# Optimization experiments

Hardware: AMD Instinct MI355X
Metric: run time of the kernel (lower is better)

Reference implementation:

```python
import jax, jax.numpy as jnp
import numpy as np

PI = 3.141592653589793


def conv2d(x, w, b=None, padding=0, groups=1):
    out = jax.lax.conv_general_dilated(
        x, w, window_strides=(1, 1), padding=((padding, padding), (padding, padding)),
        dimension_numbers=('NCHW', 'OIHW', 'NCHW'), feature_group_count=groups)
    if b is not None:
        out = out + b.reshape(1, -1, 1, 1)
    return out


def group_norm(x, weight, bias, num_groups, eps=1e-5):
    B, C, H, W = x.shape
    xg = x.reshape(B, num_groups, C // num_groups, H, W)
    mean = xg.mean(axis=(2, 3, 4), keepdims=True)
    var = xg.var(axis=(2, 3, 4), keepdims=True)
    xg = (xg - mean) / jnp.sqrt(var + eps)
    return xg.reshape(B, C, H, W) * weight.reshape(1, -1, 1, 1) + bias.reshape(1, -1, 1, 1)


def l2norm(x, eps=1e-12):
    n = jnp.sqrt(jnp.sum(x * x, axis=1, keepdims=True))
    return x / jnp.maximum(n, eps)


def dense_sift(x):
    # kornia DenseSIFTDescriptor defaults: 8 angle bins, 4x4 spatial bins, bin size 4,
    # stride 1, padding 1, rootsift=True, clipval=0.2. Input (B,1,H,W) -> (B,128,H,W).
    eps = 1e-10
    B, C, H, W = x.shape
    # spatial_gradient(x, 'diff'), normalized: central differences / 2, replicate pad
    p = jnp.pad(x, ((0, 0), (0, 0), (1, 1), (1, 1)), mode='edge')
    gx = (p[:, :, 1:-1, 2:] - p[:, :, 1:-1, :-2]) * 0.5
    gy = (p[:, :, 2:, 1:-1] - p[:, :, :-2, 1:-1]) * 0.5
    mag = jnp.sqrt(gx * gx + gy * gy + eps)
    ori = jnp.arctan2(gy, gx + eps) + 2.0 * PI
    o_big = 8.0 * ori / (2.0 * PI)
    bo0f = jnp.floor(o_big)
    wo1 = o_big - bo0f
    bo0 = bo0f % 8
    bo1 = (bo0 + 1) % 8
    wo0m = (1.0 - wo1) * mag
    wo1m = wo1 * mag
    bins = jnp.arange(8, dtype=x.dtype).reshape(1, 8, 1, 1)
    # soft orientation-histogram binning -> (B,8,H,W)
    ang = jnp.where(bo0 == bins, wo0m, 0.0) + jnp.where(bo1 == bins, wo1m, 0.0)
    # triangular bin pooling kernel (ksize=4), depthwise conv, pad 2 -> (B,8,H+1,W+1)
    ks2 = 2.0
    xc2 = ks2 - jnp.abs(jnp.arange(4, dtype=x.dtype) + 0.5 - ks2)
    pk = jnp.outer(xc2, xc2) / (ks2 ** 2)
    pk = jnp.tile(pk.reshape(1, 1, 4, 4), (8, 1, 1, 1))
    pooled = jax.lax.conv_general_dilated(
        ang, pk, (1, 1), ((2, 2), (2, 2)),
        dimension_numbers=('NCHW', 'OIHW', 'NCHW'), feature_group_count=8)
    # PoolingConv with identity reshape kernel (k=4, pad=1) == 4x4 patch extraction
    pp = jnp.pad(pooled, ((0, 0), (0, 0), (1, 1), (1, 1)))
    patches = jnp.stack([pp[:, :, y:y + H, xx:xx + W]
                         for y in range(4) for xx in range(4)], axis=2)  # (B,8,16,H,W)
    out = patches.reshape(B, 128, H, W)
    out = jnp.clip(l2norm(out), 0.0, 0.2)
    out = l2norm(out)
    # rootsift: sqrt(L1-normalized + eps)
    l1 = jnp.sum(jnp.abs(out), axis=1, keepdims=True)
    out = jnp.sqrt(out / jnp.maximum(l1, 1e-12) + eps)
    return out


def gauss1d(ks, sigma):
    t = jnp.arange(ks, dtype=jnp.float32) - (ks - 1) / 2.0
    g = jnp.exp(-(t * t) / (2.0 * sigma * sigma))
    return g / g.sum()


def joint_bilateral_blur(inp, guidance, ks=5, sigma_color=0.1, sigma_space=(1.5, 1.5)):
    # kornia joint_bilateral_blur: border_type='reflect', color_distance_type='l1'
    B, C, H, W = inp.shape
    pad = ks // 2
    pi_ = jnp.pad(inp, ((0, 0), (0, 0), (pad, pad), (pad, pad)), mode='reflect')
    pg = jnp.pad(guidance, ((0, 0), (0, 0), (pad, pad), (pad, pad)), mode='reflect')

    def unfold(p):  # (B,C,H,W,ks*ks), flatten order (dy, dx)
        return jnp.stack([p[:, :, y:y + H, x:x + W]
                          for y in range(ks) for x in range(ks)], axis=-1)

    ui = unfold(pi_)
    ug = unfold(pg)
    diff = ug - guidance[..., None]
    cdist_sq = jnp.square(jnp.sum(jnp.abs(diff), axis=1, keepdims=True))  # L1 over channels, squared
    color_k = jnp.exp(-0.5 / (sigma_color ** 2) * cdist_sq)               # (B,1,H,W,K2)
    space_k = jnp.outer(gauss1d(ks, sigma_space[0]), gauss1d(ks, sigma_space[1])).reshape(1, 1, 1, 1, -1)
    kernel = space_k * color_k
    return (ui * kernel).sum(-1) / kernel.sum(-1)


def setup_inputs() -> dict:
    key = jax.random.key(0)
    ks = jax.random.split(key, 8)
    B, H, W = 4, 270, 512

    def wgt(k, shape, scale=0.05):
        return jax.random.normal(k, shape, dtype=jnp.float32) * scale

    z = lambda n: jnp.zeros((n,), dtype=jnp.float32)
    o = lambda n: jnp.ones((n,), dtype=jnp.float32)
    return {
        'x': jax.random.normal(ks[0], (B, 1, H, W), dtype=jnp.float32),
        'w1': wgt(ks[1], (64, 128, 5, 5)), 'b1': z(64), 'g1w': o(64), 'g1b': z(64),
        'w2': wgt(ks[2], (32, 64, 3, 3)), 'b2': z(32), 'g2w': o(32), 'g2b': z(32),
        'w3': wgt(ks[3], (16, 32, 3, 3)), 'b3': z(16), 'g3w': o(16), 'g3b': z(16),
        'w4': wgt(ks[4], (8, 16, 3, 3)), 'b4': z(8), 'g4w': o(8), 'g4b': z(8),
        'w5': wgt(ks[5], (2, 8, 3, 3)), 'b5': z(2),
        'sw1': wgt(ks[6], (32, 128, 1, 1)), 'sb1': z(32),
        'sw2': wgt(ks[7], (8, 32, 1, 1)), 'sb2': z(8),
    }


def reference(x, w1, b1, g1w, g1b, w2, b2, g2w, g2b, w3, b3, g3w, g3b,
              w4, b4, g4w, g4b, w5, b5, sw1, sb1, sw2, sb2):
    orig = x
    s = dense_sift(x)                                     # (B,128,H,W)
    h = jax.nn.relu(group_norm(conv2d(s, w1, b1, 2), g1w, g1b, 8))
    h = jax.nn.relu(group_norm(conv2d(h, w2, b2, 1), g2w, g2b, 8))
    h = h + conv2d(s, sw1, sb1, 0)                        # skip 1
    blk = h
    h = jax.nn.relu(group_norm(conv2d(h, w3, b3, 1), g3w, g3b, 4))
    h = jax.nn.relu(group_norm(conv2d(h, w4, b4, 1), g4w, g4b, 4))
    h = h + conv2d(blk, sw2, sb2, 0)                      # skip 2
    h = conv2d(h, w5, b5, 1)                              # (B,2,H,W)
    guide = jnp.tile(orig, (1, 2, 1, 1))
    h = joint_bilateral_blur(h, guide, ks=5, sigma_color=0.1, sigma_space=(1.5, 1.5))
    h = jnp.tanh(h)
    scale = jnp.array([0.436, 0.615], dtype=h.dtype).reshape(1, 2, 1, 1)
    return h * scale
```

## Files before the change

### kernel.cpp

```cpp
#include <hip/hip_runtime.h>

#define DEV __device__ __forceinline__

typedef __bf16 bf16x8 __attribute__((ext_vector_type(8)));
typedef float f32x4 __attribute__((ext_vector_type(4)));

union U8 { uint4 q; unsigned short u[8]; };

constexpr int BN = 4, H = 270, W = 512, HW = H * W;
constexpr int IH5 = 274, P5 = 516;
constexpr int IH3 = 272, P3 = 514;

DEV unsigned short f2bf(float f) {
  unsigned int u = __builtin_bit_cast(unsigned int, f);
  u = (u + 0x7FFFu + ((u >> 16) & 1u)) >> 16;
  return (unsigned short)u;
}
DEV float bf2f(unsigned short h) {
  return __builtin_bit_cast(float, (unsigned int)h << 16);
}

#define GLL16(g, l)                                                                        \
  __builtin_amdgcn_global_load_lds((const __attribute__((address_space(1))) void*)(g),     \
                                   (__attribute__((address_space(3))) void*)(l), 16, 0, 0)

DEV int swz(int row) { return ((row >> 1) & 3) << 4; }

__global__ void k_fill(float* __restrict__ out, int n, float v) {
  int i = blockIdx.x * 256 + threadIdx.x;
  if (i < n) out[i] = v;
}

template <int C, int PD>
__global__ void k_halo(unsigned short* __restrict__ buf, int IHt, int pitch, int nb_) {
  int vPerRow = pitch * C / 8;
  int topBot = 2 * PD * vPerRow;
  int sideV = PD * C / 8;
  int midRows = IHt - 2 * PD;
  int perS = topBot + midRows * 2 * sideV;
  int v = blockIdx.x * 256 + threadIdx.x;
  if (v >= nb_ * perS) return;
  int s = v / perS, r = v % perS;
  size_t base = (size_t)s * IHt * pitch * C;
  size_t off;
  if (r < topBot) {
    int half = r / (PD * vPerRow);
    int rr = r % (PD * vPerRow);
    off = ((size_t)(half ? (IHt - PD) : 0) * pitch * C) + (size_t)rr * 8;
  } else {
    int r2 = r - topBot;
    int row = r2 / (2 * sideV), c2 = r2 % (2 * sideV);
    int side = c2 / sideV, cc = c2 % sideV;
    off = ((size_t)(PD + row) * pitch + (side ? (pitch - PD) : 0)) * C + (size_t)cc * 8;
  }
  *(uint4*)(buf + base + off) = uint4{0, 0, 0, 0};
}

__global__ void k_sift_ang(const float* __restrict__ x, float* __restrict__ ang, int nTot) {
  int p = blockIdx.x * 256 + threadIdx.x;
  if (p >= nTot) return;
  int b = p / HW, r = p % HW, y = r / W, xx = r % W;
  const float* xb = x + (size_t)b * HW;
  float xm = xb[y * W + (xx > 0 ? xx - 1 : 0)];
  float xp = xb[y * W + (xx < W - 1 ? xx + 1 : W - 1)];
  float ym = xb[(y > 0 ? y - 1 : 0) * W + xx];
  float yp = xb[(y < H - 1 ? y + 1 : H - 1) * W + xx];
  float gx = (xp - xm) * 0.5f, gy = (yp - ym) * 0.5f;
  float mag = sqrtf(gx * gx + gy * gy + 1e-10f);
  float ori = atan2f(gy, gx + 1e-10f) + 6.2831855f;
  float o = (8.0f * ori) / 6.2831855f;
  float bo0f = floorf(o);
  float wo1 = o - bo0f;
  int b0 = ((int)bo0f) & 7;
  int b1 = (b0 + 1) & 7;
  float w0m = (1.0f - wo1) * mag, w1m = wo1 * mag;
  float v[8];
#pragma unroll
  for (int k = 0; k < 8; ++k)
    v[k] = (k == b0 ? w0m : 0.0f) + (k == b1 ? w1m : 0.0f);
  float4* o4 = (float4*)(ang + (size_t)p * 8);
  o4[0] = make_float4(v[0], v[1], v[2], v[3]);
  o4[1] = make_float4(v[4], v[5], v[6], v[7]);
}

__global__ void k_sift_pool(const float* __restrict__ ang, float* __restrict__ pooled, int nTot) {
  constexpr int PH = H + 1, PW = W + 1;
  int p = blockIdx.x * 256 + threadIdx.x;
  if (p >= nTot) return;
  int b = p / (PH * PW), r = p % (PH * PW), y = r / PW, xx = r % PW;
  float4 a0 = {0, 0, 0, 0}, a1 = {0, 0, 0, 0};
  const float xc2[4] = {0.5f, 1.5f, 1.5f, 0.5f};
#pragma unroll
  for (int ky = 0; ky < 4; ++ky) {
    int yy = y - 2 + ky;
    if (yy < 0 || yy >= H) continue;
#pragma unroll
    for (int kx = 0; kx < 4; ++kx) {
      int xs = xx - 2 + kx;
      if (xs < 0 || xs >= W) continue;
      float w = xc2[ky] * xc2[kx] * 0.25f;
      const float4* s4 = (const float4*)(ang + ((size_t)(b * H + yy) * W + xs) * 8);
      float4 v0 = s4[0], v1 = s4[1];
      a0.x += w * v0.x; a0.y += w * v0.y; a0.z += w * v0.z; a0.w += w * v0.w;
      a1.x += w * v1.x; a1.y += w * v1.y; a1.z += w * v1.z; a1.w += w * v1.w;
    }
  }
  float4* o4 = (float4*)(pooled + (size_t)p * 8);
  o4[0] = a0; o4[1] = a1;
}

__global__ void k_sift_desc(const float* __restrict__ pooled, unsigned short* __restrict__ spad) {
  constexpr int PH = H + 1, PW = W + 1;
  int tid = threadIdx.x;
  int wv = tid >> 6, lane = tid & 63;
  int p = blockIdx.x * 4 + wv;
  int b = p / HW, r = p % HW, yy = r / W, xx = r % W;
  int a = lane >> 3, jj = lane & 7;
  int j0 = jj * 2;
  int dy = j0 >> 2, dx = j0 & 3;
  int rr = yy + dy - 1;
  int c0 = xx + dx - 1, c1 = c0 + 1;
  bool rv = (rr >= 0 && rr <= H);
  int rc = min(max(rr, 0), H);
  const float* pb = pooled + ((size_t)(b * PH + rc) * PW) * 8 + a;
  float v0 = 0.0f, v1 = 0.0f;
  if (rv && c0 >= 0 && c0 <= W) v0 = pb[(size_t)c0 * 8];
  if (rv && c1 >= 0 && c1 <= W) v1 = pb[(size_t)c1 * 8];

  float n2 = v0 * v0 + v1 * v1;
#pragma unroll
  for (int m = 1; m < 64; m <<= 1) n2 += __shfl_xor(n2, m);
  float inv = 1.0f / fmaxf(sqrtf(n2), 1e-12f);
  v0 = fminf(v0 * inv, 0.2f);
  v1 = fminf(v1 * inv, 0.2f);
  float S = v0 + v1;
#pragma unroll
  for (int m = 1; m < 64; m <<= 1) S += __shfl_xor(S, m);
  float iS = 1.0f / fmaxf(S, 1e-12f);
  v0 = sqrtf(v0 * iS + 1e-10f);
  v1 = sqrtf(v1 * iS + 1e-10f);
  unsigned int pk = (unsigned int)f2bf(v0) | ((unsigned int)f2bf(v1) << 16);
  *(unsigned int*)(spad + ((size_t)(b * IH5 + yy + 2) * P5 + xx + 2) * 128 + lane * 2) = pk;
}

template <int CIN, int COUT, int KS>
__global__ void k_prep(const float* __restrict__ w, unsigned short* __restrict__ wbuf) {
  int i = blockIdx.x * 256 + threadIdx.x;
  if (i >= KS * KS * COUT * CIN) return;
  int t = i / (COUT * CIN), r2 = i % (COUT * CIN), co = r2 / CIN, e = r2 % CIN;
  wbuf[i] = f2bf(w[(co * CIN + e) * (KS * KS) + t]);
}

DEV int xcd_remap(int bid, int nbid) {
  int q8 = nbid >> 3, r8 = nbid & 7;
  int xcd = bid & 7;
  return (xcd < r8 ? xcd * (q8 + 1) : r8 * (q8 + 1) + (xcd - r8) * q8) + (bid >> 3);
}

template <int CIN, int COUT, int KS, int NG, int MINW, bool FSKIP, int BMPX>
__launch_bounds__(BMPX, MINW)
__global__ void k_convr(const unsigned short* __restrict__ in, int IHt, int ipitch,
                        const unsigned short* __restrict__ wtap,
                        const float* __restrict__ bias,
                        const unsigned short* __restrict__ wsk,
                        const float* __restrict__ skb,
                        unsigned short* __restrict__ outraw,
                        unsigned short* __restrict__ skraw,
                        float* __restrict__ part, int nbid) {
  constexpr int NWV = BMPX / 64;
  constexpr int NXB = 512 / BMPX;
  constexpr int SLABPX = BMPX + KS - 1;
  constexpr int KQ = CIN / 32;
  constexpr int NF = COUT / 16;
  constexpr int SLAB = SLABPX * 64;
  constexpr int SWQ = COUT * 64;
  constexpr int SWROW = KS * SWQ;
  constexpr int SSK = FSKIP ? 32 * 64 : 16;
  constexpr int STRIDE = BMPX * 16;
  __shared__ __align__(16) unsigned char slabB[2][SLAB];
  __shared__ __align__(16) unsigned char wrowB[2][SWROW];
  __shared__ __align__(16) unsigned char wskB[2][SSK];
  __shared__ float red[NWV][16];

  int tid = threadIdx.x;
  int lane = tid & 63, wid = tid >> 6;
  int l15 = lane & 15, hi = lane >> 4;

  int byl = xcd_remap(blockIdx.x, nbid);
  int half = byl % NXB, rowid = byl / NXB;
  int y = rowid % H, b = rowid / H;
  int x0 = half * BMPX;

  f32x4 acc[4][NF] = {};
  f32x4 ask[4][2] = {};

  auto stage = [&](int it, int pbuf) {
    int q = it / KS, ky = it % KS;
    const char* src = (const char*)(in + ((size_t)(b * IHt + y + ky) * ipitch + x0) * CIN + q * 32);
    for (int d = tid * 16; d < SLAB; d += STRIDE) {
      int px = d >> 6, qb = d & 63;
      GLL16(src + px * (CIN * 2) + (qb ^ swz(px)), slabB[pbuf] + d);
    }
    const char* wsrc = (const char*)wtap + (size_t)(ky * KS) * (COUT * CIN * 2) + q * 64;
    for (int d = tid * 16; d < SWROW; d += STRIDE) {
      int kx = d / SWQ, rem = d % SWQ;
      int co = rem >> 6, qb = rem & 63;
      GLL16(wsrc + (size_t)kx * (COUT * CIN * 2) + co * (CIN * 2) + (qb ^ swz(co)), wrowB[pbuf] + d);
    }
  };
  auto stage_wsk = [&](int q, int pbuf) {
    const char* src = (const char*)wsk + q * 64;
    for (int d = tid * 16; d < 32 * 64; d += STRIDE) {
      int co = d >> 6, qb = d & 63;
      GLL16(src + co * (CIN * 2) + (qb ^ swz(co)), wskB[pbuf] + d);
    }
  };

  stage(0, 0);
  if constexpr (FSKIP) stage_wsk(0, 0);
  __syncthreads();

#pragma unroll 1
  for (int it = 0; it < KQ * KS; ++it) {
    int cur = it & 1;
    int q = it / KS, ky = it % KS;
    if (it + 1 < KQ * KS) {
      stage(it + 1, cur ^ 1);
      if (FSKIP && (it + 1) % KS == 0) stage_wsk((it + 1) / KS, ((it + 1) / KS) & 1);
    }
    const unsigned char* sl = slabB[cur];
    const unsigned char* wr = wrowB[cur];
    int koff = hi * 16;
#pragma unroll
    for (int kx = 0; kx < KS; ++kx) {
      bf16x8 af[4];
#pragma unroll
      for (int mi = 0; mi < 4; ++mi) {
        int px = wid * 64 + mi * 16 + l15 + kx;
        af[mi] = *(const bf16x8*)(sl + px * 64 + (koff ^ swz(px)));
      }
#pragma unroll
      for (int ni = 0; ni < NF; ++ni) {
        int co = ni * 16 + l15;
        bf16x8 bq = *(const bf16x8*)(wr + kx * SWQ + co * 64 + (koff ^ swz(co)));
#pragma unroll
        for (int mi = 0; mi < 4; ++mi)
          acc[mi][ni] = __builtin_amdgcn_mfma_f32_16x16x32_bf16(af[mi], bq, acc[mi][ni], 0, 0, 0);
      }
      if constexpr (FSKIP) {
        if (ky == KS / 2 && kx == KS / 2) {
#pragma unroll
          for (int ni = 0; ni < 2; ++ni) {
            int co = ni * 16 + l15;
            bf16x8 bq = *(const bf16x8*)(wskB[q & 1] + co * 64 + (koff ^ swz(co)));
#pragma unroll
            for (int mi = 0; mi < 4; ++mi)
              ask[mi][ni] = __builtin_amdgcn_mfma_f32_16x16x32_bf16(af[mi], bq, ask[mi][ni], 0, 0, 0);
          }
        }
      }
    }
    __syncthreads();
  }

#pragma unroll
  for (int ni = 0; ni < NF; ++ni) {
    float bv = bias[ni * 16 + l15];
#pragma unroll
    for (int mi = 0; mi < 4; ++mi)
#pragma unroll
      for (int rr = 0; rr < 4; ++rr)
        acc[mi][ni][rr] += bv;
  }
  unsigned short* op = outraw + ((size_t)(b * H + y) * W + x0) * COUT;
#pragma unroll
  for (int mi = 0; mi < 4; ++mi)
#pragma unroll
    for (int rr = 0; rr < 4; ++rr) {
      int px = wid * 64 + mi * 16 + hi * 4 + rr;
#pragma unroll
      for (int ni = 0; ni < NF; ++ni)
        op[(size_t)px * COUT + ni * 16 + l15] = f2bf(acc[mi][ni][rr]);
    }
  if constexpr (FSKIP) {
    unsigned short* ops = skraw + ((size_t)(b * H + y) * W + x0) * 32;
#pragma unroll
    for (int ni = 0; ni < 2; ++ni) {
      float bv = skb[ni * 16 + l15];
#pragma unroll
      for (int mi = 0; mi < 4; ++mi)
#pragma unroll
        for (int rr = 0; rr < 4; ++rr)
          ask[mi][ni][rr] += bv;
    }
#pragma unroll
    for (int mi = 0; mi < 4; ++mi)
#pragma unroll
      for (int rr = 0; rr < 4; ++rr) {
        int px = wid * 64 + mi * 16 + hi * 4 + rr;
#pragma unroll
        for (int ni = 0; ni < 2; ++ni)
          ops[(size_t)px * 32 + ni * 16 + l15] = f2bf(ask[mi][ni][rr]);
      }
  }
  if constexpr (NG > 0) {
    constexpr int GPC = COUT / NG;
#pragma unroll
    for (int ni = 0; ni < NF; ++ni) {
      float s = 0.0f, q2 = 0.0f;
#pragma unroll
      for (int mi = 0; mi < 4; ++mi)
#pragma unroll
        for (int rr = 0; rr < 4; ++rr) {
          float v = acc[mi][ni][rr];
          s += v; q2 += v * v;
        }
      s += __shfl_xor(s, 16); q2 += __shfl_xor(q2, 16);
      s += __shfl_xor(s, 32); q2 += __shfl_xor(q2, 32);
#pragma unroll
      for (int m = 1; m < GPC; m <<= 1) { s += __shfl_xor(s, m); q2 += __shfl_xor(q2, m); }
      if (hi == 0 && (l15 % GPC) == 0) {
        int g = ni * (16 / GPC) + l15 / GPC;
        red[wid][g] = s;
        red[wid][NG + g] = q2;
      }
    }
    __syncthreads();
    if (tid < 2 * NG) {
      float t = 0.0f;
#pragma unroll
      for (int wv2 = 0; wv2 < NWV; ++wv2) t += red[wv2][tid];
      part[(size_t)byl * (2 * NG) + tid] = t;
    }
  }
}

template <int COUT, int NG>
__global__ void k_gn_fin(const float* __restrict__ part, int NB,
                         const float* __restrict__ gw, const float* __restrict__ gb,
                         float* __restrict__ scale, float* __restrict__ shift, float invN) {
  constexpr int GPC = COUT / NG;
  int b = blockIdx.x / NG, g = blockIdx.x % NG;
  int lane = threadIdx.x;
  float s = 0.0f, q = 0.0f;
  for (int i = lane; i < NB; i += 64) {
    const float* pp = part + (size_t)(b * NB + i) * (2 * NG);
    s += pp[g]; q += pp[NG + g];
  }
#pragma unroll
  for (int m = 1; m < 64; m <<= 1) { s += __shfl_xor(s, m); q += __shfl_xor(q, m); }
  if (lane == 0) {
    float mean = s * invN;
    float var = q * invN - mean * mean;
    float rstd = rsqrtf(var + 1e-5f);
#pragma unroll
    for (int j = 0; j < GPC; ++j) {
      int c = g * GPC + j;
      float sc = gw[c] * rstd;
      scale[b * COUT + c] = sc;
      shift[b * COUT + c] = gb[c] - mean * sc;
    }
  }
}

template <int C, bool ADDSKIP>
__global__ void k_norm(const unsigned short* __restrict__ raw,
                       const unsigned short* __restrict__ skip,
                       const float* __restrict__ scale, const float* __restrict__ shift,
                       unsigned short* __restrict__ outpad) {
  int e = blockIdx.x * 256 + threadIdx.x;
  int idx = e * 8;
  int p = idx / C, c0 = idx % C;
  int b = p / HW, r = p % HW, y = r / W, xx = r % W;
  U8 v; v.q = *(const uint4*)(raw + (size_t)p * C + c0);
  U8 sk;
  if (ADDSKIP) sk.q = *(const uint4*)(skip + (size_t)p * C + c0);
  const float* sc = scale + b * C + c0;
  const float* sh = shift + b * C + c0;
  U8 o;
#pragma unroll
  for (int j = 0; j < 8; ++j) {
    float f = fmaxf(bf2f(v.u[j]) * sc[j] + sh[j], 0.0f);
    if (ADDSKIP) f += bf2f(sk.u[j]);
    o.u[j] = f2bf(f);
  }
  *(uint4*)(outpad + ((size_t)(b * IH3 + y + 1) * P3 + xx + 1) * C + c0) = o.q;
}

__global__ void k_conv4(const unsigned short* __restrict__ h3raw, const float* __restrict__ w4,
                        const float* __restrict__ b4,
                        const float* __restrict__ sc3, const float* __restrict__ sh3,
                        unsigned short* __restrict__ h4raw, float* __restrict__ part) {
  __shared__ float wl[1152];
  __shared__ float scs[16], shs[16];
  __shared__ float red[4][8];
  int b0 = (blockIdx.x * 256) / HW;
  for (int i = threadIdx.x; i < 1152; i += 256) {
    int t = i / 128, r2 = i % 128, ci = r2 >> 3, co = r2 & 7;
    wl[i] = w4[(co * 16 + ci) * 9 + t];
  }
  if (threadIdx.x < 16) { scs[threadIdx.x] = sc3[b0 * 16 + threadIdx.x]; shs[threadIdx.x] = sh3[b0 * 16 + threadIdx.x]; }
  __syncthreads();
  int p = blockIdx.x * 256 + threadIdx.x;
  int b = p / HW, r = p % HW, y = r / W, xx = r % W;
  float acc[8];
#pragma unroll
  for (int co = 0; co < 8; ++co) acc[co] = b4[co];
#pragma unroll
  for (int t = 0; t < 9; ++t) {
    int ky = t / 3, kx = t % 3;
    int row = y + ky - 1, x = xx + kx - 1;
    if (row < 0 || row >= H || x < 0 || x >= W) continue;
    const unsigned short* ip = h3raw + ((size_t)(b * H + row) * W + x) * 16;
    U8 u0, u1;
    u0.q = *(const uint4*)ip;
    u1.q = *(const uint4*)(ip + 8);
#pragma unroll
    for (int ci = 0; ci < 16; ++ci) {
      float raw = bf2f(ci < 8 ? u0.u[ci] : u1.u[ci - 8]);
      float iv = fmaxf(raw * scs[ci] + shs[ci], 0.0f);
#pragma unroll
      for (int co = 0; co < 8; ++co)
        acc[co] += iv * wl[t * 128 + ci * 8 + co];
    }
  }
  int lane = threadIdx.x & 63, wv = threadIdx.x >> 6;
  float s[4], q[4];
#pragma unroll
  for (int g = 0; g < 4; ++g) {
    s[g] = acc[2 * g] + acc[2 * g + 1];
    q[g] = acc[2 * g] * acc[2 * g] + acc[2 * g + 1] * acc[2 * g + 1];
  }
#pragma unroll
  for (int m = 1; m < 64; m <<= 1) {
#pragma unroll
    for (int g = 0; g < 4; ++g) { s[g] += __shfl_xor(s[g], m); q[g] += __shfl_xor(q[g], m); }
  }
  if (lane == 0) {
#pragma unroll
    for (int g = 0; g < 4; ++g) { red[wv][g] = s[g]; red[wv][4 + g] = q[g]; }
  }
  __syncthreads();
  if (threadIdx.x < 8)
    part[(size_t)blockIdx.x * 8 + threadIdx.x] =
        red[0][threadIdx.x] + red[1][threadIdx.x] + red[2][threadIdx.x] + red[3][threadIdx.x];
  U8 o;
#pragma unroll
  for (int co = 0; co < 8; ++co) o.u[co] = f2bf(acc[co]);
  *(uint4*)(h4raw + (size_t)p * 8) = o.q;
}

__global__ void k_norm4(const unsigned short* __restrict__ h4raw, const unsigned short* __restrict__ blkpad,
                        const float* __restrict__ scale, const float* __restrict__ shift,
                        const float* __restrict__ sw2, const float* __restrict__ sb2,
                        unsigned short* __restrict__ blk2pad) {
  __shared__ float wl[256];
  {
    int i = threadIdx.x;
    int ci = i >> 3, co = i & 7;
    wl[i] = sw2[co * 32 + ci];
  }
  __syncthreads();
  int p = blockIdx.x * 256 + threadIdx.x;
  int b = p / HW, r = p % HW, y = r / W, xx = r % W;
  float acc[8];
#pragma unroll
  for (int co = 0; co < 8; ++co) acc[co] = sb2[co];
  size_t cbase = ((size_t)(b * IH3 + y + 1) * P3 + (xx + 1));
  const unsigned short* bp = blkpad + cbase * 32;
#pragma unroll
  for (int half = 0; half < 4; ++half) {
    U8 u; u.q = *(const uint4*)(bp + half * 8);
#pragma unroll
    for (int j = 0; j < 8; ++j) {
      float iv = bf2f(u.u[j]);
      int ci = half * 8 + j;
#pragma unroll
      for (int co = 0; co < 8; ++co) acc[co] += iv * wl[ci * 8 + co];
    }
  }
  U8 hv; hv.q = *(const uint4*)(h4raw + (size_t)p * 8);
  U8 o;
#pragma unroll
  for (int co = 0; co < 8; ++co) {
    float f = fmaxf(bf2f(hv.u[co]) * scale[b * 8 + co] + shift[b * 8 + co], 0.0f) + acc[co];
    o.u[co] = f2bf(f);
  }
  *(uint4*)(blk2pad + cbase * 8) = o.q;
}

__global__ void k_conv5(const unsigned short* __restrict__ blk2pad, const float* __restrict__ w5,
                        const float* __restrict__ b5, float* __restrict__ h5) {
  __shared__ float wl[144];
  if (threadIdx.x < 144) {
    int i = threadIdx.x;
    int t = i / 16, r2 = i % 16, ci = r2 >> 1, co = r2 & 1;
    wl[i] = w5[(co * 8 + ci) * 9 + t];
  }
  __syncthreads();
  int p = blockIdx.x * 256 + threadIdx.x;
  int b = p / HW, r = p % HW, y = r / W, xx = r % W;
  float a0 = b5[0], a1 = b5[1];
#pragma unroll
  for (int t = 0; t < 9; ++t) {
    int ky = t / 3, kx = t % 3;
    const unsigned short* ip = blk2pad + ((size_t)(b * IH3 + y + ky) * P3 + (xx + kx)) * 8;
    U8 u; u.q = *(const uint4*)ip;
#pragma unroll
    for (int ci = 0; ci < 8; ++ci) {
      float iv = bf2f(u.u[ci]);
      a0 += iv * wl[t * 16 + ci * 2];
      a1 += iv * wl[t * 16 + ci * 2 + 1];
    }
  }
  h5[(size_t)p * 2] = a0;
  h5[(size_t)p * 2 + 1] = a1;
}

__global__ void k_bilateral(const float* __restrict__ h5, const float* __restrict__ x,
                            float* __restrict__ out, int nTot) {
  int p = blockIdx.x * 256 + threadIdx.x;
  if (p >= nTot) return;
  int b = p / HW, r = p % HW, y = r / W, xx = r % W;
  const float* xb = x + (size_t)b * HW;
  float xc = xb[r];
  float e1 = expf(-1.0f / 4.5f), e0 = expf(-4.0f / 4.5f);
  float gs = 1.0f + 2.0f * e1 + 2.0f * e0;
  float g[5] = {e0 / gs, e1 / gs, 1.0f / gs, e1 / gs, e0 / gs};
  float n0 = 0.0f, n1 = 0.0f, den = 0.0f;
#pragma unroll
  for (int dy = 0; dy < 5; ++dy) {
    int yn = y + dy - 2;
    yn = yn < 0 ? -yn : (yn >= H ? 2 * H - 2 - yn : yn);
#pragma unroll
    for (int dx = 0; dx < 5; ++dx) {
      int xn = xx + dx - 2;
      xn = xn < 0 ? -xn : (xn >= W ? 2 * W - 2 - xn : xn);
      float xv = xb[yn * W + xn];
      float d = xv - xc;
      float wgt = g[dy] * g[dx] * expf(-200.0f * d * d);
      den += wgt;
      const float* hp = h5 + ((size_t)(b * HW) + yn * W + xn) * 2;
      n0 += wgt * hp[0];
      n1 += wgt * hp[1];
    }
  }
  float o0 = tanhf(n0 / den) * 0.436f;
  float o1 = tanhf(n1 / den) * 0.615f;
  out[(size_t)(b * 2) * HW + r] = o0;
  out[(size_t)(b * 2 + 1) * HW + r] = o1;
}

extern "C" void kernel_launch(void* const* d_in, const int* in_sizes, int n_in,
                              void* d_out, int out_size, void* d_ws, size_t ws_size,
                              hipStream_t stream) {
  (void)in_sizes; (void)n_in; (void)out_size;
  const float* x   = (const float*)d_in[0];
  const float* w1  = (const float*)d_in[1];
  const float* b1  = (const float*)d_in[2];
  const float* g1w = (const float*)d_in[3];
  const float* g1b = (const float*)d_in[4];
  const float* w2  = (const float*)d_in[5];
  const float* b2  = (const float*)d_in[6];
  const float* g2w = (const float*)d_in[7];
  const float* g2b = (const float*)d_in[8];
  const float* w3  = (const float*)d_in[9];
  const float* b3  = (const float*)d_in[10];
  const float* g3w = (const float*)d_in[11];
  const float* g3b = (const float*)d_in[12];
  const float* w4  = (const float*)d_in[13];
  const float* b4  = (const float*)d_in[14];
  const float* g4w = (const float*)d_in[15];
  const float* g4b = (const float*)d_in[16];
  const float* w5  = (const float*)d_in[17];
  const float* b5  = (const float*)d_in[18];
  const float* sw1 = (const float*)d_in[19];
  const float* sb1 = (const float*)d_in[20];
  const float* sw2 = (const float*)d_in[21];
  const float* sb2 = (const float*)d_in[22];
  float* out = (float*)d_out;
  char* ws = (char*)d_ws;

  auto AL = [](size_t v) { return (v + 255) & ~(size_t)255; };
  const size_t sSPAD  = (size_t)IH5 * P5 * 128 * 2;
  const size_t sANG   = (size_t)HW * 8 * 4;
  const size_t sH1RAW = (size_t)HW * 64 * 2;
  const size_t sH1PAD = (size_t)IH3 * P3 * 64 * 2;
  const size_t sH2RAW = (size_t)HW * 32 * 2;
  const size_t sBLKP  = (size_t)IH3 * P3 * 32 * 2;
  const size_t sH3RAW = (size_t)HW * 16 * 2;
  const size_t sH3PAD = (size_t)IH3 * P3 * 16 * 2;
  const size_t sH4RAW = (size_t)HW * 8 * 2;
  const size_t sBLK2  = (size_t)IH3 * P3 * 8 * 2;

  int nb = 0;
  size_t offB = 0, offH1PAD = 0, offSmall = 0;
  const size_t smallFixed = AL(1024 * 1024) + AL((size_t)4 * 1080 * 16 * 4) + 8 * 4096;
  for (int cand = 4; cand >= 1; cand >>= 1) {
    size_t oB   = AL((size_t)cand * sSPAD);
    size_t oH1P = AL(oB + (size_t)cand * sH1RAW);
    size_t oS   = AL(oH1P + (size_t)cand * sH1PAD);
    size_t need = oS + smallFixed + AL((size_t)cand * sH2RAW);
    if (ws_size >= need) { nb = cand; offB = oB; offH1PAD = oH1P; offSmall = oS; break; }
  }
  if (nb == 0) {
    k_fill<<<(BN * 2 * HW + 255) / 256, 256, 0, stream>>>(out, BN * 2 * HW, 123.0f);
    return;
  }

  size_t oWB1  = offSmall;
  size_t oWB2  = AL(oWB1 + 25 * 64 * 128 * 2);
  size_t oWB3  = AL(oWB2 + 9 * 32 * 64 * 2);
  size_t oWBS  = AL(oWB3 + 9 * 16 * 32 * 2);
  size_t oPART = AL(oWBS + 32 * 128 * 2);
  size_t oSC1  = AL(oPART + (size_t)4 * 1080 * 16 * 4);
  size_t oSC2  = oSC1 + 4096, oSC3 = oSC2 + 4096, oSC4 = oSC3 + 4096;
  size_t oSK1  = oSC4 + 4096;

  unsigned short* wb1  = (unsigned short*)(ws + oWB1);
  unsigned short* wb2  = (unsigned short*)(ws + oWB2);
  unsigned short* wb3  = (unsigned short*)(ws + oWB3);
  unsigned short* wbs1 = (unsigned short*)(ws + oWBS);
  float* part = (float*)(ws + oPART);
  float* sc1 = (float*)(ws + oSC1); float* sh1 = sc1 + nb * 64;
  float* sc2 = (float*)(ws + oSC2); float* sh2 = sc2 + nb * 32;
  float* sc3 = (float*)(ws + oSC3); float* sh3 = sc3 + nb * 16;
  float* sc4 = (float*)(ws + oSC4); float* sh4 = sc4 + nb * 8;
  unsigned short* sk1 = (unsigned short*)(ws + oSK1);

  k_prep<128, 64, 5><<<800, 256, 0, stream>>>(w1, wb1);
  k_prep<64, 32, 3><<<72, 256, 0, stream>>>(w2, wb2);
  k_prep<32, 16, 3><<<18, 256, 0, stream>>>(w3, wb3);
  k_prep<128, 32, 1><<<16, 256, 0, stream>>>(sw1, wbs1);

  size_t t0 = AL((size_t)nb * sBLKP);
  size_t t1 = AL(t0 + (size_t)nb * sH3RAW);
  size_t t2 = AL(t1 + (size_t)nb * sH3PAD);
  size_t t3 = AL(t2 + (size_t)nb * sH4RAW);
  size_t t4 = AL(t3 + (size_t)nb * sBLK2);

  for (int b0 = 0; b0 < BN; b0 += nb) {
    const float* x_c = x + (size_t)b0 * HW;
    float* out_c = out + (size_t)b0 * 2 * HW;
    unsigned short* spad   = (unsigned short*)(ws);
    float*          ang    = (float*)(ws + offB);
    float*          pooled = (float*)(ws + AL(offB + (size_t)nb * sANG));
    unsigned short* h1raw  = (unsigned short*)(ws + offB);
    unsigned short* h1pad  = (unsigned short*)(ws + offH1PAD);
    unsigned short* h2raw  = (unsigned short*)(ws + offB);
    unsigned short* blkpad = (unsigned short*)(ws);
    unsigned short* h3raw  = (unsigned short*)(ws + t0);
    unsigned short* h4raw  = (unsigned short*)(ws + t2);
    unsigned short* blk2   = (unsigned short*)(ws + t3);
    float*          h5     = (float*)(ws + t4);
    int nHW = nb * HW;

    k_halo<128, 2><<<(nb * 50304 + 255) / 256, 256, 0, stream>>>(spad, IH5, P5, nb);
    k_halo<64, 1><<<(nb * 12544 + 255) / 256, 256, 0, stream>>>(h1pad, IH3, P3, nb);

    k_sift_ang<<<nb * 540, 256, 0, stream>>>(x_c, ang, nHW);
    int nPP = nb * (H + 1) * (W + 1);
    k_sift_pool<<<(nPP + 255) / 256, 256, 0, stream>>>(ang, pooled, nPP);
    k_sift_desc<<<nHW / 4, 256, 0, stream>>>(pooled, spad);

    int n1 = nb * H * 2;
    k_convr<128, 64, 5, 8, 2, true, 256><<<n1, 256, 0, stream>>>(
        spad, IH5, P5, wb1, b1, wbs1, sb1, h1raw, sk1, part, n1);
    k_gn_fin<64, 8><<<nb * 8, 64, 0, stream>>>(part, 2 * H, g1w, g1b, sc1, sh1, 1.0f / (8.0f * HW));
    k_norm<64, false><<<nb * 4320, 256, 0, stream>>>(h1raw, nullptr, sc1, sh1, h1pad);

    int n2 = nb * H;
    k_convr<64, 32, 3, 8, 4, false, 512><<<n2, 512, 0, stream>>>(
        h1pad, IH3, P3, wb2, b2, nullptr, nullptr, h2raw, nullptr, part, n2);
    k_gn_fin<32, 8><<<nb * 8, 64, 0, stream>>>(part, H, g2w, g2b, sc2, sh2, 1.0f / (4.0f * HW));

    k_halo<32, 1><<<(nb * 6272 + 255) / 256, 256, 0, stream>>>(blkpad, IH3, P3, nb);
    k_halo<8, 1><<<(nb * 1568 + 255) / 256, 256, 0, stream>>>(blk2, IH3, P3, nb);

    k_norm<32, true><<<nb * 2160, 256, 0, stream>>>(h2raw, sk1, sc2, sh2, blkpad);

    k_convr<32, 16, 3, 4, 4, false, 512><<<n2, 512, 0, stream>>>(
        blkpad, IH3, P3, wb3, b3, nullptr, nullptr, h3raw, nullptr, part, n2);
    k_gn_fin<16, 4><<<nb * 4, 64, 0, stream>>>(part, H, g3w, g3b, sc3, sh3, 1.0f / (4.0f * HW));

    k_conv4<<<nb * 540, 256, 0, stream>>>(h3raw, w4, b4, sc3, sh3, h4raw, part);
    k_gn_fin<8, 4><<<nb * 4, 64, 0, stream>>>(part, 540, g4w, g4b, sc4, sh4, 1.0f / (2.0f * HW));

    k_norm4<<<nb * 540, 256, 0, stream>>>(h4raw, blkpad, sc4, sh4, sw2, sb2, blk2);

    k_conv5<<<nb * 540, 256, 0, stream>>>(blk2, w5, b5, h5);
    k_bilateral<<<nb * 540, 256, 0, stream>>>(h5, x_c, out_c, nHW);
  }
}
```

Before: 664.0 us.

## Fuse GroupNorm+ReLU(+skip) into conv2/conv3 input staging, drop padded buffers

Adds a new MFMA conv kernel that reads the raw previous-layer output, applies the GroupNorm scale/shift, ReLU and optional skip add while staging rows into LDS, and zero-fills out-of-range pixels itself. This removes the standalone normalize kernels, the padded intermediate buffers and their halo-fill launches for conv2 and conv3. The final 1x1 skip in k_norm4 now recomputes the normalized block activation from h2raw and sk1 instead of reading a stored copy. The cost is extra ALU work per staged element, since each input row is normalized once per kernel-row tap, and a different staging and pipelining scheme than the previous conv kernel.

```diff
diff --git a/kernel.cpp b/kernel.cpp
--- a/kernel.cpp
+++ b/kernel.cpp
@@ -335,6 +335,150 @@
   }
 }
 
+template <int CIN, int COUT, int KS, int NG, bool ADDSK>
+__launch_bounds__(512, 4)
+__global__ void k_convf(const unsigned short* __restrict__ in,
+                        const unsigned short* __restrict__ skin,
+                        const unsigned short* __restrict__ wtap,
+                        const float* __restrict__ bias,
+                        const float* __restrict__ scg, const float* __restrict__ shg,
+                        unsigned short* __restrict__ outraw,
+                        float* __restrict__ part, int nbid) {
+  constexpr int SLABPX = 512 + KS - 1;
+  constexpr int KQ = CIN / 32;
+  constexpr int NF = COUT / 16;
+  constexpr int SLAB = SLABPX * 64;
+  constexpr int SWQ = COUT * 64;
+  constexpr int SWROW = KS * SWQ;
+  __shared__ __align__(16) unsigned char slabB[2][SLAB];
+  __shared__ __align__(16) unsigned char wrowB[2][SWROW];
+  __shared__ float scS[CIN], shS[CIN];
+  __shared__ float red[8][16];
+
+  int tid = threadIdx.x;
+  int lane = tid & 63, wid = tid >> 6;
+  int l15 = lane & 15, hi = lane >> 4;
+
+  int byl = xcd_remap(blockIdx.x, nbid);
+  int y = byl % H, b = byl / H;
+
+  if (tid < CIN) { scS[tid] = scg[b * CIN + tid]; shS[tid] = shg[b * CIN + tid]; }
+  __syncthreads();
+
+  f32x4 acc[4][NF] = {};
+
+  auto stage = [&](int it, int pbuf) {
+    int q = it / KS, ky = it % KS;
+    int row = y + ky - 1;
+    bool rowok = (row >= 0 && row < H);
+    for (int d = tid * 16; d < SLAB; d += 8192) {
+      int px = d >> 6, qb = d & 63;
+      int x = px - 1;
+      U8 o; o.q = uint4{0, 0, 0, 0};
+      if (rowok && x >= 0 && x < W) {
+        size_t e = ((size_t)(b * H + row) * W + x) * CIN + q * 32;
+        U8 u; u.q = *(const uint4*)((const char*)in + e * 2 + qb);
+        U8 s;
+        if (ADDSK) s.q = *(const uint4*)((const char*)skin + e * 2 + qb);
+        int cb = q * 32 + (qb >> 1);
+#pragma unroll
+        for (int j = 0; j < 8; ++j) {
+          float f = fmaxf(bf2f(u.u[j]) * scS[cb + j] + shS[cb + j], 0.0f);
+          if (ADDSK) f += bf2f(s.u[j]);
+          o.u[j] = f2bf(f);
+        }
+      }
+      *(uint4*)(slabB[pbuf] + px * 64 + (qb ^ swz(px))) = o.q;
+    }
+    const char* wsrc = (const char*)wtap + (size_t)(ky * KS) * (COUT * CIN * 2) + q * 64;
+    for (int d = tid * 16; d < SWROW; d += 8192) {
+      int kx = d / SWQ, rem = d % SWQ;
+      int co = rem >> 6, qb = rem & 63;
+      GLL16(wsrc + (size_t)kx * (COUT * CIN * 2) + co * (CIN * 2) + (qb ^ swz(co)), wrowB[pbuf] + d);
+    }
+  };
+
+  stage(0, 0);
+  __syncthreads();
+
+#pragma unroll 1
+  for (int it = 0; it < KQ * KS; ++it) {
+    int cur = it & 1;
+    if (it + 1 < KQ * KS) stage(it + 1, cur ^ 1);
+    const unsigned char* sl = slabB[cur];
+    const unsigned char* wr = wrowB[cur];
+    int koff = hi * 16;
+#pragma unroll
+    for (int kx = 0; kx < KS; ++kx) {
+      bf16x8 af[4];
+#pragma unroll
+      for (int mi = 0; mi < 4; ++mi) {
+        int px = wid * 64 + mi * 16 + l15 + kx;
+        af[mi] = *(const bf16x8*)(sl + px * 64 + (koff ^ swz(px)));
+      }
+#pragma unroll
+      for (int ni = 0; ni < NF; ++ni) {
+        int co = ni * 16 + l15;
+        bf16x8 bq = *(const bf16x8*)(wr + kx * SWQ + co * 64 + (koff ^ swz(co)));
+#pragma unroll
+        for (int mi = 0; mi < 4; ++mi)
+          acc[mi][ni] = __builtin_amdgcn_mfma_f32_16x16x32_bf16(af[mi], bq, acc[mi][ni], 0, 0, 0);
+      }
+    }
+    __syncthreads();
+  }
+
+#pragma unroll
+  for (int ni = 0; ni < NF; ++ni) {
+    float bv = bias[ni * 16 + l15];
+#pragma unroll
+    for (int mi = 0; mi < 4; ++mi)
+#pragma unroll
+      for (int rr = 0; rr < 4; ++rr)
+        acc[mi][ni][rr] += bv;
+  }
+  unsigned short* op = outraw + ((size_t)(b * H + y) * W) * COUT;
+#pragma unroll
+  for (int mi = 0; mi < 4; ++mi)
+#pragma unroll
+    for (int rr = 0; rr < 4; ++rr) {
+      int px = wid * 64 + mi * 16 + hi * 4 + rr;
+#pragma unroll
+      for (int ni = 0; ni < NF; ++ni)
+        op[(size_t)px * COUT + ni * 16 + l15] = f2bf(acc[mi][ni][rr]);
+    }
+  if constexpr (NG > 0) {
+    constexpr int GPC = COUT / NG;
+#pragma unroll
+    for (int ni = 0; ni < NF; ++ni) {
+      float s = 0.0f, q2 = 0.0f;
+#pragma unroll
+      for (int mi = 0; mi < 4; ++mi)
+#pragma unroll
+        for (int rr = 0; rr < 4; ++rr) {
+          float v = acc[mi][ni][rr];
+          s += v; q2 += v * v;
+        }
+      s += __shfl_xor(s, 16); q2 += __shfl_xor(q2, 16);
+      s += __shfl_xor(s, 32); q2 += __shfl_xor(q2, 32);
+#pragma unroll
+      for (int m = 1; m < GPC; m <<= 1) { s += __shfl_xor(s, m); q2 += __shfl_xor(q2, m); }
+      if (hi == 0 && (l15 % GPC) == 0) {
+        int g = ni * (16 / GPC) + l15 / GPC;
+        red[wid][g] = s;
+        red[wid][NG + g] = q2;
+      }
+    }
+    __syncthreads();
+    if (tid < 2 * NG) {
+      float t = 0.0f;
+#pragma unroll
+      for (int wv2 = 0; wv2 < 8; ++wv2) t += red[wv2][tid];
+      part[(size_t)byl * (2 * NG) + tid] = t;
+    }
+  }
+}
+
 template <int COUT, int NG>
 __global__ void k_gn_fin(const float* __restrict__ part, int NB,
                          const float* __restrict__ gw, const float* __restrict__ gb,
@@ -363,30 +507,6 @@
   }
 }
 
-template <int C, bool ADDSKIP>
-__global__ void k_norm(const unsigned short* __restrict__ raw,
-                       const unsigned short* __restrict__ skip,
-                       const float* __restrict__ scale, const float* __restrict__ shift,
-                       unsigned short* __restrict__ outpad) {
-  int e = blockIdx.x * 256 + threadIdx.x;
-  int idx = e * 8;
-  int p = idx / C, c0 = idx % C;
-  int b = p / HW, r = p % HW, y = r / W, xx = r % W;
-  U8 v; v.q = *(const uint4*)(raw + (size_t)p * C + c0);
-  U8 sk;
-  if (ADDSKIP) sk.q = *(const uint4*)(skip + (size_t)p * C + c0);
-  const float* sc = scale + b * C + c0;
-  const float* sh = shift + b * C + c0;
-  U8 o;
-#pragma unroll
-  for (int j = 0; j < 8; ++j) {
-    float f = fmaxf(bf2f(v.u[j]) * sc[j] + sh[j], 0.0f);
-    if (ADDSKIP) f += bf2f(sk.u[j]);
-    o.u[j] = f2bf(f);
-  }
-  *(uint4*)(outpad + ((size_t)(b * IH3 + y + 1) * P3 + xx + 1) * C + c0) = o.q;
-}
-
 __global__ void k_conv4(const unsigned short* __restrict__ h3raw, const float* __restrict__ w4,
                         const float* __restrict__ b4,
                         const float* __restrict__ sc3, const float* __restrict__ sh3,
@@ -450,15 +570,21 @@
   *(uint4*)(h4raw + (size_t)p * 8) = o.q;
 }
 
-__global__ void k_norm4(const unsigned short* __restrict__ h4raw, const unsigned short* __restrict__ blkpad,
-                        const float* __restrict__ scale, const float* __restrict__ shift,
+__global__ void k_norm4(const unsigned short* __restrict__ h4raw,
+                        const unsigned short* __restrict__ h2raw,
+                        const unsigned short* __restrict__ sk1,
+                        const float* __restrict__ sc2, const float* __restrict__ sh2,
+                        const float* __restrict__ sc4, const float* __restrict__ sh4,
                         const float* __restrict__ sw2, const float* __restrict__ sb2,
                         unsigned short* __restrict__ blk2pad) {
   __shared__ float wl[256];
+  __shared__ float s2[32], h2s[32];
+  int b0 = (blockIdx.x * 256) / HW;
   {
     int i = threadIdx.x;
     int ci = i >> 3, co = i & 7;
     wl[i] = sw2[co * 32 + ci];
+    if (i < 32) { s2[i] = sc2[b0 * 32 + i]; h2s[i] = sh2[b0 * 32 + i]; }
   }
   __syncthreads();
   int p = blockIdx.x * 256 + threadIdx.x;
@@ -466,26 +592,28 @@
   float acc[8];
 #pragma unroll
   for (int co = 0; co < 8; ++co) acc[co] = sb2[co];
-  size_t cbase = ((size_t)(b * IH3 + y + 1) * P3 + (xx + 1));
-  const unsigned short* bp = blkpad + cbase * 32;
+  const unsigned short* hp2 = h2raw + (size_t)p * 32;
+  const unsigned short* skp = sk1 + (size_t)p * 32;
 #pragma unroll
   for (int half = 0; half < 4; ++half) {
-    U8 u; u.q = *(const uint4*)(bp + half * 8);
+    U8 u; u.q = *(const uint4*)(hp2 + half * 8);
+    U8 s; s.q = *(const uint4*)(skp + half * 8);
 #pragma unroll
     for (int j = 0; j < 8; ++j) {
-      float iv = bf2f(u.u[j]);
       int ci = half * 8 + j;
-#pragma unroll
-      for (int co = 0; co < 8; ++co) acc[co] += iv * wl[ci * 8 + co];
+      float blk = fmaxf(bf2f(u.u[j]) * s2[ci] + h2s[ci], 0.0f) + bf2f(s.u[j]);
+#pragma unroll
+      for (int co = 0; co < 8; ++co) acc[co] += blk * wl[ci * 8 + co];
     }
   }
   U8 hv; hv.q = *(const uint4*)(h4raw + (size_t)p * 8);
   U8 o;
 #pragma unroll
   for (int co = 0; co < 8; ++co) {
-    float f = fmaxf(bf2f(hv.u[co]) * scale[b * 8 + co] + shift[b * 8 + co], 0.0f) + acc[co];
+    float f = fmaxf(bf2f(hv.u[co]) * sc4[b * 8 + co] + sh4[b * 8 + co], 0.0f) + acc[co];
     o.u[co] = f2bf(f);
   }
+  size_t cbase = ((size_t)(b * IH3 + y + 1) * P3 + (xx + 1));
   *(uint4*)(blk2pad + cbase * 8) = o.q;
 }
 
@@ -587,21 +715,19 @@
   const size_t sH1RAW = (size_t)HW * 64 * 2;
   const size_t sH1PAD = (size_t)IH3 * P3 * 64 * 2;
   const size_t sH2RAW = (size_t)HW * 32 * 2;
-  const size_t sBLKP  = (size_t)IH3 * P3 * 32 * 2;
   const size_t sH3RAW = (size_t)HW * 16 * 2;
-  const size_t sH3PAD = (size_t)IH3 * P3 * 16 * 2;
   const size_t sH4RAW = (size_t)HW * 8 * 2;
   const size_t sBLK2  = (size_t)IH3 * P3 * 8 * 2;
 
   int nb = 0;
-  size_t offB = 0, offH1PAD = 0, offSmall = 0;
+  size_t offB = 0, offSmall = 0;
   const size_t smallFixed = AL(1024 * 1024) + AL((size_t)4 * 1080 * 16 * 4) + 8 * 4096;
   for (int cand = 4; cand >= 1; cand >>= 1) {
     size_t oB   = AL((size_t)cand * sSPAD);
     size_t oH1P = AL(oB + (size_t)cand * sH1RAW);
     size_t oS   = AL(oH1P + (size_t)cand * sH1PAD);
     size_t need = oS + smallFixed + AL((size_t)cand * sH2RAW);
-    if (ws_size >= need) { nb = cand; offB = oB; offH1PAD = oH1P; offSmall = oS; break; }
+    if (ws_size >= need) { nb = cand; offB = oB; offSmall = oS; break; }
   }
   if (nb == 0) {
     k_fill<<<(BN * 2 * HW + 255) / 256, 256, 0, stream>>>(out, BN * 2 * HW, 123.0f);
@@ -633,11 +759,10 @@
   k_prep<32, 16, 3><<<18, 256, 0, stream>>>(w3, wb3);
   k_prep<128, 32, 1><<<16, 256, 0, stream>>>(sw1, wbs1);
 
-  size_t t0 = AL((size_t)nb * sBLKP);
-  size_t t1 = AL(t0 + (size_t)nb * sH3RAW);
-  size_t t2 = AL(t1 + (size_t)nb * sH3PAD);
-  size_t t3 = AL(t2 + (size_t)nb * sH4RAW);
-  size_t t4 = AL(t3 + (size_t)nb * sBLK2);
+  size_t u0 = AL((size_t)nb * sH2RAW);
+  size_t u1 = AL(u0 + (size_t)nb * sH3RAW);
+  size_t u2 = AL(u1 + (size_t)nb * sH4RAW);
+  size_t u3 = AL(u2 + (size_t)nb * sBLK2);
 
   for (int b0 = 0; b0 < BN; b0 += nb) {
     const float* x_c = x + (size_t)b0 * HW;
@@ -646,17 +771,14 @@
     float*          ang    = (float*)(ws + offB);
     float*          pooled = (float*)(ws + AL(offB + (size_t)nb * sANG));
     unsigned short* h1raw  = (unsigned short*)(ws + offB);
-    unsigned short* h1pad  = (unsigned short*)(ws + offH1PAD);
-    unsigned short* h2raw  = (unsigned short*)(ws + offB);
-    unsigned short* blkpad = (unsigned short*)(ws);
-    unsigned short* h3raw  = (unsigned short*)(ws + t0);
-    unsigned short* h4raw  = (unsigned short*)(ws + t2);
-    unsigned short* blk2   = (unsigned short*)(ws + t3);
-    float*          h5     = (float*)(ws + t4);
+    unsigned short* h2raw  = (unsigned short*)(ws);
+    unsigned short* h3raw  = (unsigned short*)(ws + u0);
+    unsigned short* h4raw  = (unsigned short*)(ws + u1);
+    unsigned short* blk2   = (unsigned short*)(ws + u2);
+    float*          h5     = (float*)(ws + u3);
     int nHW = nb * HW;
 
     k_halo<128, 2><<<(nb * 50304 + 255) / 256, 256, 0, stream>>>(spad, IH5, P5, nb);
-    k_halo<64, 1><<<(nb * 12544 + 255) / 256, 256, 0, stream>>>(h1pad, IH3, P3, nb);
 
     k_sift_ang<<<nb * 540, 256, 0, stream>>>(x_c, ang, nHW);
     int nPP = nb * (H + 1) * (W + 1);
@@ -667,26 +789,21 @@
     k_convr<128, 64, 5, 8, 2, true, 256><<<n1, 256, 0, stream>>>(
         spad, IH5, P5, wb1, b1, wbs1, sb1, h1raw, sk1, part, n1);
     k_gn_fin<64, 8><<<nb * 8, 64, 0, stream>>>(part, 2 * H, g1w, g1b, sc1, sh1, 1.0f / (8.0f * HW));
-    k_norm<64, false><<<nb * 4320, 256, 0, stream>>>(h1raw, nullptr, sc1, sh1, h1pad);
 
     int n2 = nb * H;
-    k_convr<64, 32, 3, 8, 4, false, 512><<<n2, 512, 0, stream>>>(
-        h1pad, IH3, P3, wb2, b2, nullptr, nullptr, h2raw, nullptr, part, n2);
+    k_convf<64, 32, 3, 8, false><<<n2, 512, 0, stream>>>(
+        h1raw, nullptr, wb2, b2, sc1, sh1, h2raw, part, n2);
     k_gn_fin<32, 8><<<nb * 8, 64, 0, stream>>>(part, H, g2w, g2b, sc2, sh2, 1.0f / (4.0f * HW));
 
-    k_halo<32, 1><<<(nb * 6272 + 255) / 256, 256, 0, stream>>>(blkpad, IH3, P3, nb);
-    k_halo<8, 1><<<(nb * 1568 + 255) / 256, 256, 0, stream>>>(blk2, IH3, P3, nb);
-
-    k_norm<32, true><<<nb * 2160, 256, 0, stream>>>(h2raw, sk1, sc2, sh2, blkpad);
-
-    k_convr<32, 16, 3, 4, 4, false, 512><<<n2, 512, 0, stream>>>(
-        blkpad, IH3, P3, wb3, b3, nullptr, nullptr, h3raw, nullptr, part, n2);
+    k_convf<32, 16, 3, 4, true><<<n2, 512, 0, stream>>>(
+        h2raw, sk1, wb3, b3, sc2, sh2, h3raw, part, n2);
     k_gn_fin<16, 4><<<nb * 4, 64, 0, stream>>>(part, H, g3w, g3b, sc3, sh3, 1.0f / (4.0f * HW));
 
     k_conv4<<<nb * 540, 256, 0, stream>>>(h3raw, w4, b4, sc3, sh3, h4raw, part);
     k_gn_fin<8, 4><<<nb * 4, 64, 0, stream>>>(part, 540, g4w, g4b, sc4, sh4, 1.0f / (2.0f * HW));
 
-    k_norm4<<<nb * 540, 256, 0, stream>>>(h4raw, blkpad, sc4, sh4, sw2, sb2, blk2);
+    k_halo<8, 1><<<(nb * 1568 + 255) / 256, 256, 0, stream>>>(blk2, IH3, P3, nb);
+    k_norm4<<<nb * 540, 256, 0, stream>>>(h4raw, h2raw, sk1, sc2, sh2, sc4, sh4, sw2, sb2, blk2);
 
     k_conv5<<<nb * 540, 256, 0, stream>>>(blk2, w5, b5, h5);
     k_bilateral<<<nb * 540, 256, 0, stream>>>(h5, x_c, out_c, nHW);
```

After: 673.1 us. Within noise of the previous version (+1.4%).
